# Kernel optimization log

Measured on AMD Instinct MI355X. Metric: run time of the kernel, lower is better.

## Reference

```python
import jax, jax.numpy as jnp
import numpy as np

N_SUM, N_MAX, M, HID, OUT, E, L = 2048, 64, 16, 128, 64, 16384, 4


def setup_inputs() -> dict:
    key = jax.random.key(0)
    ks = jax.random.split(key, 8)
    inp = {}
    inp["W"] = jax.random.normal(ks[0], (N_SUM, N_MAX, M), jnp.float32)
    inp["mask"] = jnp.ones((N_SUM, N_MAX), jnp.float32)
    inp["src"] = jax.random.randint(ks[1], (E,), 0, N_SUM)
    inp["dst"] = jax.random.randint(ks[2], (E,), 0, N_SUM)
    # GIN parameters: per-layer eps, MLP (Linear -> BN -> ReLU -> Linear)
    inp["eps"] = jax.random.normal(ks[3], (L,), jnp.float32)
    inp["W1_first"] = jax.random.normal(ks[4], (M, HID), jnp.float32) / np.sqrt(M).astype(np.float32)
    inp["b1_first"] = jnp.zeros((HID,), jnp.float32)
    inp["W1_rest"] = jax.random.normal(ks[5], (L - 1, HID, HID), jnp.float32) / np.sqrt(HID).astype(np.float32)
    inp["b1_rest"] = jnp.zeros((L - 1, HID), jnp.float32)
    inp["bn_gamma"] = jnp.ones((L, HID), jnp.float32)
    inp["bn_beta"] = jnp.zeros((L, HID), jnp.float32)
    inp["W2_mid"] = jax.random.normal(ks[6], (L - 1, HID, HID), jnp.float32) / np.sqrt(HID).astype(np.float32)
    inp["b2_mid"] = jnp.zeros((L - 1, HID), jnp.float32)
    inp["W2_last"] = jax.random.normal(ks[7], (HID, OUT), jnp.float32) / np.sqrt(HID).astype(np.float32)
    inp["b2_last"] = jnp.zeros((OUT,), jnp.float32)
    return inp


def _batchnorm(Hf, gamma, beta):
    # training-mode BatchNorm1d over flattened leading dims (biased variance)
    mu = Hf.mean(axis=0)
    var = Hf.var(axis=0)
    return (Hf - mu) * jax.lax.rsqrt(var + 1e-5) * gamma + beta


def _gin_layer(X, src, dst, eps, W1, b1, gamma, beta, W2, b2):
    # scatter-add message passing: gather sources, segment-sum into targets
    S = jax.ops.segment_sum(X[src], dst, num_segments=X.shape[0])  # [N_sum, n_max, D]
    Z = (1.0 + eps) * X + S
    H = Z @ W1 + b1                     # [N_sum, n_max, HID]
    shp = H.shape
    H = _batchnorm(H.reshape(-1, shp[-1]), gamma, beta)
    H = jax.nn.relu(H).reshape(shp)
    return H @ W2 + b2


def reference(W, mask, src, dst, eps, W1_first, b1_first, W1_rest, b1_rest,
              bn_gamma, bn_beta, W2_mid, b2_mid, W2_last, b2_last):
    X = W
    for l in range(L):
        W1 = W1_first if l == 0 else W1_rest[l - 1]
        b1 = b1_first if l == 0 else b1_rest[l - 1]
        W2 = W2_mid[l] if l < L - 1 else W2_last
        b2 = b2_mid[l] if l < L - 1 else b2_last
        X = _gin_layer(X, src, dst, eps[l], W1, b1, bn_gamma[l], bn_beta[l], W2, b2)
    # masked sum over the padded node axis -> positional encodings [N_sum, OUT]
    PE = (X * mask[:, :, None]).sum(axis=1)
    return PE
```

## Files before the change

kernel.cpp:

```cpp
#include <hip/hip_runtime.h>

#define N_SUM 2048
#define HIDD 128
#define NEDGE 16384
#define ROWS (N_SUM * 64)
#define NSLOT 16

typedef short short8 __attribute__((ext_vector_type(8)));
typedef float floatx4 __attribute__((ext_vector_type(4)));
typedef unsigned int uint4n __attribute__((ext_vector_type(4)));
typedef unsigned short ushort_t;

__device__ __forceinline__ ushort_t f2bf(float f) {
    unsigned u = __builtin_bit_cast(unsigned, f);
    u += 0x7fffu + ((u >> 16) & 1u);
    return (ushort_t)(u >> 16);
}
__device__ __forceinline__ float bf2f(ushort_t h) {
    return __builtin_bit_cast(float, (unsigned)h << 16);
}
__device__ __forceinline__ void unpack8(uint4 v, float* f) {
    f[0] = bf2f(v.x & 0xffff); f[1] = bf2f(v.x >> 16);
    f[2] = bf2f(v.y & 0xffff); f[3] = bf2f(v.y >> 16);
    f[4] = bf2f(v.z & 0xffff); f[5] = bf2f(v.z >> 16);
    f[6] = bf2f(v.w & 0xffff); f[7] = bf2f(v.w >> 16);
}
__device__ __forceinline__ uint4 pack8(const float* f) {
    uint4 v;
    v.x = f2bf(f[0]) | ((unsigned)f2bf(f[1]) << 16);
    v.y = f2bf(f[2]) | ((unsigned)f2bf(f[3]) << 16);
    v.z = f2bf(f[4]) | ((unsigned)f2bf(f[5]) << 16);
    v.w = f2bf(f[6]) | ((unsigned)f2bf(f[7]) << 16);
    return v;
}
__device__ __forceinline__ void nt_store16(const void* src, void* dst) {
    __builtin_nontemporal_store(*(const uint4n*)src, (uint4n*)dst);
}

__global__ __launch_bounds__(256) void zero_ints(int* p, int n) {
    int i = blockIdx.x * 256 + threadIdx.x;
    if (i < n) p[i] = 0;
}

__global__ __launch_bounds__(256) void count_deg(const int* __restrict__ dst, int* __restrict__ deg) {
    int e = blockIdx.x * 256 + threadIdx.x;
    if (e < NEDGE) atomicAdd(&deg[dst[e]], 1);
}

__global__ __launch_bounds__(256) void scan_deg(const int* __restrict__ deg, int* __restrict__ row_ptr) {
    __shared__ int csum[256];
    int t = threadIdx.x;
    int loc[8];
    int s = 0;
#pragma unroll
    for (int q = 0; q < 8; q++) { loc[q] = s; s += deg[t * 8 + q]; }
    csum[t] = s;
    __syncthreads();
    for (int off = 1; off < 256; off <<= 1) {
        int v = (t >= off) ? csum[t - off] : 0;
        __syncthreads();
        csum[t] += v;
        __syncthreads();
    }
    int base = (t == 0) ? 0 : csum[t - 1];
#pragma unroll
    for (int q = 0; q < 8; q++) row_ptr[t * 8 + q] = base + loc[q];
    if (t == 255) row_ptr[2048] = csum[255];
}

__global__ __launch_bounds__(256) void fill_csr(const int* __restrict__ src, const int* __restrict__ dst,
                                                const int* __restrict__ row_ptr, int* __restrict__ cursor,
                                                int* __restrict__ col) {
    int e = blockIdx.x * 256 + threadIdx.x;
    if (e < NEDGE) {
        int d = dst[e];
        int pos = atomicAdd(&cursor[d], 1);
        col[row_ptr[d] + pos] = src[e];
    }
}

__global__ __launch_bounds__(256) void prep_small(const float* __restrict__ W1f, const float* __restrict__ W2l,
                                                  const float* __restrict__ b2m, const float* __restrict__ W1r,
                                                  ushort_t* __restrict__ w1t0, ushort_t* __restrict__ w2lt,
                                                  float* __restrict__ bvec) {
    int idx = blockIdx.x * 256 + threadIdx.x;
    if (idx < 4096) {
        int nn = idx >> 5, k = idx & 31;
        w1t0[idx] = f2bf(k < 16 ? W1f[k * 128 + nn] : 0.f);
    } else if (idx < 4096 + 8192) {
        int r = idx - 4096;
        int nn = r >> 7, k = r & 127;
        w2lt[r] = f2bf(W2l[k * 64 + nn]);
    } else if (idx < 4096 + 8192 + 384) {
        int r = idx - 12288;
        int lm = r >> 7, c = r & 127;
        float s = 0.f;
        for (int o = 0; o < 128; o++) s += b2m[lm * 128 + o] * W1r[(size_t)lm * 16384 + o * 128 + c];
        bvec[r] = s;
    }
}

__global__ __launch_bounds__(256) void prep_w21(const float* __restrict__ W2m, const float* __restrict__ W1r,
                                                ushort_t* __restrict__ w21t) {
    int idx = blockIdx.x * 256 + threadIdx.x;
    int lm = idx >> 14, r = idx & 16383, i = r >> 7, c = r & 127;
    const float* w2row = W2m + (size_t)lm * 16384 + i * 128;
    const float* w1col = W1r + (size_t)lm * 16384 + c;
    float s = 0.f;
#pragma unroll 8
    for (int o = 0; o < 128; o++) s += w2row[o] * w1col[o * 128];
    w21t[(size_t)lm * 16384 + c * 128 + i] = f2bf(s);
}


__global__ __launch_bounds__(256, 4) void gin_mm1_l0(const float* __restrict__ Xf, const ushort_t* __restrict__ W1t,
                                                     const float* __restrict__ b1, const float* __restrict__ eps,
                                                     const int* __restrict__ rp, const int* __restrict__ colv,
                                                     ushort_t* __restrict__ H, float* __restrict__ sums) {
    __shared__ ushort_t Zs[64 * 128];
    int tid = threadIdx.x, n = blockIdx.x;
    float ev = 1.0f + eps[0];
    int e0 = rp[n], e1 = rp[n + 1], deg = e1 - e0;
    const float4* X = (const float4*)Xf;

    float4 sA, sB;
    sA = X[(size_t)n * 256 + tid];
    if (deg > 0) sB = X[(size_t)colv[e0] * 256 + tid];
    float4 a;
    a.x = sA.x * ev; a.y = sA.y * ev; a.z = sA.z * ev; a.w = sA.w * ev;
    int i = 1;
    for (; i + 1 < deg; i += 2) {
        sA = X[(size_t)colv[e0 + i] * 256 + tid];
        a.x += sB.x; a.y += sB.y; a.z += sB.z; a.w += sB.w;
        sB = X[(size_t)colv[e0 + i + 1] * 256 + tid];
        a.x += sA.x; a.y += sA.y; a.z += sA.z; a.w += sA.w;
    }
    if (deg > 0) {
        if (i < deg) {
            sA = X[(size_t)colv[e0 + i] * 256 + tid];
            a.x += sB.x; a.y += sB.y; a.z += sB.z; a.w += sB.w;
            a.x += sA.x; a.y += sA.y; a.z += sA.z; a.w += sA.w;
        } else {
            a.x += sB.x; a.y += sB.y; a.z += sB.z; a.w += sB.w;
        }
    }

    {
        int m = tid >> 2, k0 = (tid & 3) * 4;
        int addr = ((k0 >> 3) * 64 + m) * 8 + (k0 & 7);
        uint2 pv;
        pv.x = f2bf(a.x) | ((unsigned)f2bf(a.y) << 16);
        pv.y = f2bf(a.z) | ((unsigned)f2bf(a.w) << 16);
        *(uint2*)&Zs[addr] = pv;
        *(uint2*)&Zs[1024 + tid * 4] = make_uint2(0u, 0u);
    }
    __syncthreads();

    int w = tid >> 6, lane = tid & 63, lg = lane >> 4, ln = lane & 15;
    floatx4 C[4][2];
#pragma unroll
    for (int mt = 0; mt < 4; mt++) { C[mt][0] = {0.f, 0.f, 0.f, 0.f}; C[mt][1] = {0.f, 0.f, 0.f, 0.f}; }

    {
        short8 B0 = *(const short8*)&W1t[(w * 32 + ln) * 32 + lg * 8];
        short8 B1 = *(const short8*)&W1t[(w * 32 + 16 + ln) * 32 + lg * 8];
#pragma unroll
        for (int mt = 0; mt < 4; mt++) {
            short8 A = *(const short8*)&Zs[(lg * 64 + mt * 16 + ln) * 8];
            C[mt][0] = __builtin_amdgcn_mfma_f32_16x16x32_bf16(A, B0, C[mt][0], 0, 0, 0);
            C[mt][1] = __builtin_amdgcn_mfma_f32_16x16x32_bf16(A, B1, C[mt][1], 0, 0, 0);
        }
    }

    float bsum[2], bsq[2];
    float bv[2] = {b1[w * 32 + ln], b1[w * 32 + 16 + ln]};
#pragma unroll
    for (int nt = 0; nt < 2; nt++) {
        float s = 0.f, s2 = 0.f;
#pragma unroll
        for (int mt = 0; mt < 4; mt++)
#pragma unroll
            for (int r = 0; r < 4; r++) {
                float v = C[mt][nt][r] + bv[nt];
                C[mt][nt][r] = v;
                s += v; s2 += v * v;
            }
        bsum[nt] = s; bsq[nt] = s2;
    }
#pragma unroll
    for (int nt = 0; nt < 2; nt++) {
        bsum[nt] += __shfl_xor(bsum[nt], 16, 64);
        bsum[nt] += __shfl_xor(bsum[nt], 32, 64);
        bsq[nt] += __shfl_xor(bsq[nt], 16, 64);
        bsq[nt] += __shfl_xor(bsq[nt], 32, 64);
    }
    if (lg == 0) {
        float* sl = sums + (n & (NSLOT - 1)) * 256;
        int c0 = w * 32 + ln;
        atomicAdd(&sl[c0], bsum[0]);
        atomicAdd(&sl[c0 + 16], bsum[1]);
        atomicAdd(&sl[128 + c0], bsq[0]);
        atomicAdd(&sl[128 + c0 + 16], bsq[1]);
    }
    __syncthreads();
#pragma unroll
    for (int nt = 0; nt < 2; nt++) {
        int colc = w * 32 + nt * 16 + ln;
        int base = (colc >> 3) * 512 + (colc & 7);
#pragma unroll
        for (int mt = 0; mt < 4; mt++)
#pragma unroll
            for (int r = 0; r < 4; r++) {
                int row = mt * 16 + lg * 4 + r;
                Zs[base + row * 8] = f2bf(C[mt][nt][r]);
            }
    }
    __syncthreads();
#pragma unroll
    for (int q = 0; q < 4; q++)
        nt_store16(&((const uint4*)Zs)[q * 256 + tid], &((uint4*)&H[(size_t)n * 8192])[q * 256 + tid]);
}

__global__ __launch_bounds__(512, 4) void gin_mm1_fused(const ushort_t* __restrict__ Hin,
                                                        const ushort_t* __restrict__ W21t,
                                                        const float* __restrict__ b1, const float* __restrict__ bvec,
                                                        const float* __restrict__ sums_prev,
                                                        const float* __restrict__ gam_prev,
                                                        const float* __restrict__ bet_prev,
                                                        const float* __restrict__ epsp,
                                                        const int* __restrict__ rp, const int* __restrict__ colv,
                                                        ushort_t* __restrict__ Hout, float* __restrict__ sums_cur) {
    __shared__ ushort_t Zs[64 * 128];
    __shared__ float scs_lds[256];
    int tid = threadIdx.x, n = blockIdx.x;
    if (tid < 128) {
        float s = 0.f, s2 = 0.f;
#pragma unroll
        for (int k = 0; k < NSLOT; k++) {
            s += sums_prev[k * 256 + tid];
            s2 += sums_prev[k * 256 + 128 + tid];
        }
        float mean = s * (1.f / (float)ROWS);
        float var = s2 * (1.f / (float)ROWS) - mean * mean;
        float sc = gam_prev[tid] * rsqrtf(var + 1e-5f);
        scs_lds[tid] = sc;
        scs_lds[128 + tid] = bet_prev[tid] - mean * sc;
    }
    __syncthreads();

    unsigned scp[2][8];
#pragma unroll
    for (int q = 0; q < 2; q++) {
        int cb = ((q * 512 + tid) >> 6) * 8;
#pragma unroll
        for (int j = 0; j < 8; j++)
            scp[q][j] = ((unsigned)f2bf(scs_lds[cb + j])) | ((unsigned)f2bf(scs_lds[128 + cb + j]) << 16);
    }

    float ev = 1.0f + epsp[0];
    int e0 = rp[n], e1 = rp[n + 1], deg = e1 - e0;
    const uint4* X = (const uint4*)Hin;
    float acc[2][8];
    uint4 bufA[2], bufB[2];

    auto loadslab = [&](uint4* buf, int node) {
        const uint4* p = X + (size_t)node * 1024;
        buf[0] = p[tid];
        buf[1] = p[512 + tid];
    };
    auto addp = [&](const uint4* buf) {
#pragma unroll
        for (int q = 0; q < 2; q++) {
            float f[8]; unpack8(buf[q], f);
#pragma unroll
            for (int j = 0; j < 8; j++) {
                float sc = __builtin_bit_cast(float, scp[q][j] << 16);
                float sh = __builtin_bit_cast(float, scp[q][j] & 0xffff0000u);
                acc[q][j] += fmaxf(fmaf(f[j], sc, sh), 0.f);
            }
        }
    };

    loadslab(bufA, n);
    if (deg > 0) loadslab(bufB, colv[e0]);

#pragma unroll
    for (int q = 0; q < 2; q++) {
        float f[8]; unpack8(bufA[q], f);
#pragma unroll
        for (int j = 0; j < 8; j++) {
            float sc = __builtin_bit_cast(float, scp[q][j] << 16);
            float sh = __builtin_bit_cast(float, scp[q][j] & 0xffff0000u);
            acc[q][j] = ev * fmaxf(fmaf(f[j], sc, sh), 0.f);
        }
    }

    int i = 1;
    for (; i + 1 < deg; i += 2) {
        loadslab(bufA, colv[e0 + i]);
        addp(bufB);
        loadslab(bufB, colv[e0 + i + 1]);
        addp(bufA);
    }
    if (deg > 0) {
        if (i < deg) {
            loadslab(bufA, colv[e0 + i]);
            addp(bufB);
            addp(bufA);
        } else {
            addp(bufB);
        }
    }

#pragma unroll
    for (int q = 0; q < 2; q++) ((uint4*)Zs)[q * 512 + tid] = pack8(acc[q]);
    __syncthreads();

    int w = tid >> 6, lane = tid & 63, lg = lane >> 4, ln = lane & 15;
    floatx4 C[4];
#pragma unroll
    for (int mt = 0; mt < 4; mt++) C[mt] = {0.f, 0.f, 0.f, 0.f};

    for (int kb = 0; kb < 4; kb++) {
        short8 B = *(const short8*)&W21t[(w * 16 + ln) * 128 + kb * 32 + lg * 8];
#pragma unroll
        for (int mt = 0; mt < 4; mt++) {
            short8 A = *(const short8*)&Zs[((kb * 4 + lg) * 64 + mt * 16 + ln) * 8];
            C[mt] = __builtin_amdgcn_mfma_f32_16x16x32_bf16(A, B, C[mt], 0, 0, 0);
        }
    }

    float fac = ev + (float)deg;
    int c0 = w * 16 + ln;
    float bv = b1[c0] + fac * bvec[c0];
    float s = 0.f, s2 = 0.f;
#pragma unroll
    for (int mt = 0; mt < 4; mt++)
#pragma unroll
        for (int r = 0; r < 4; r++) {
            float v = C[mt][r] + bv;
            C[mt][r] = v;
            s += v; s2 += v * v;
        }
    s += __shfl_xor(s, 16, 64);
    s += __shfl_xor(s, 32, 64);
    s2 += __shfl_xor(s2, 16, 64);
    s2 += __shfl_xor(s2, 32, 64);
    if (lg == 0) {
        float* sl = sums_cur + (n & (NSLOT - 1)) * 256;
        atomicAdd(&sl[c0], s);
        atomicAdd(&sl[128 + c0], s2);
    }

    __syncthreads();
    {
        int base = (c0 >> 3) * 512 + (c0 & 7);
#pragma unroll
        for (int mt = 0; mt < 4; mt++)
#pragma unroll
            for (int r = 0; r < 4; r++) {
                int row = mt * 16 + lg * 4 + r;
                Zs[base + row * 8] = f2bf(C[mt][r]);
            }
    }
    __syncthreads();
#pragma unroll
    for (int q = 0; q < 2; q++)
        nt_store16(&((const uint4*)Zs)[q * 512 + tid], &((uint4*)&Hout[(size_t)n * 8192])[q * 512 + tid]);
}

__global__ __launch_bounds__(256, 4) void gin_mm2_last(const ushort_t* __restrict__ H, const ushort_t* __restrict__ W2t,
                                                       const float* __restrict__ b2,
                                                       const float* __restrict__ sums_prev,
                                                       const float* __restrict__ gam_prev,
                                                       const float* __restrict__ bet_prev,
                                                       const float* __restrict__ mask, float* __restrict__ out) {
    __shared__ ushort_t Hs[64 * 128];
    __shared__ float scs_lds[256];
    int tid = threadIdx.x, n = blockIdx.x;
    if (tid < 128) {
        float s = 0.f, s2 = 0.f;
#pragma unroll
        for (int k = 0; k < NSLOT; k++) {
            s += sums_prev[k * 256 + tid];
            s2 += sums_prev[k * 256 + 128 + tid];
        }
        float mean = s * (1.f / (float)ROWS);
        float var = s2 * (1.f / (float)ROWS) - mean * mean;
        float sc = gam_prev[tid] * rsqrtf(var + 1e-5f);
        scs_lds[tid] = sc;
        scs_lds[128 + tid] = bet_prev[tid] - mean * sc;
    }
    __syncthreads();

#pragma unroll
    for (int q = 0; q < 4; q++) {
        int c = q * 256 + tid;
        uint4 v = ((const uint4*)&H[(size_t)n * 8192])[c];
        float f[8]; unpack8(v, f);
        int cb = (c >> 6) * 8;
#pragma unroll
        for (int j = 0; j < 8; j++) f[j] = fmaxf(fmaf(f[j], scs_lds[cb + j], scs_lds[128 + cb + j]), 0.f);
        ((uint4*)Hs)[c] = pack8(f);
    }
    __syncthreads();

    int w = tid >> 6, lane = tid & 63, lg = lane >> 4, ln = lane & 15;
    floatx4 C[4];
#pragma unroll
    for (int mt = 0; mt < 4; mt++) C[mt] = {0.f, 0.f, 0.f, 0.f};

    for (int kb = 0; kb < 4; kb++) {
        short8 B = *(const short8*)&W2t[(w * 16 + ln) * 128 + kb * 32 + lg * 8];
#pragma unroll
        for (int mt = 0; mt < 4; mt++) {
            short8 A = *(const short8*)&Hs[((kb * 4 + lg) * 64 + mt * 16 + ln) * 8];
            C[mt] = __builtin_amdgcn_mfma_f32_16x16x32_bf16(A, B, C[mt], 0, 0, 0);
        }
    }

    int colc = w * 16 + ln;
    float bb = b2[colc];
    float pe = 0.f;
#pragma unroll
    for (int mt = 0; mt < 4; mt++)
#pragma unroll
        for (int r = 0; r < 4; r++) {
            int row = mt * 16 + lg * 4 + r;
            pe += mask[n * 64 + row] * (C[mt][r] + bb);
        }
    pe += __shfl_xor(pe, 16, 64);
    pe += __shfl_xor(pe, 32, 64);
    if (lg == 0) out[(size_t)n * 64 + colc] = pe;
}

extern "C" void kernel_launch(void* const* d_in, const int* in_sizes, int n_in, void* d_out, int out_size,
                              void* d_ws, size_t ws_size, hipStream_t stream) {
    const float* W    = (const float*)d_in[0];
    const float* mask = (const float*)d_in[1];
    const int* src    = (const int*)d_in[2];
    const int* dst    = (const int*)d_in[3];
    const float* eps  = (const float*)d_in[4];
    const float* W1f  = (const float*)d_in[5];
    const float* b1f  = (const float*)d_in[6];
    const float* W1r  = (const float*)d_in[7];
    const float* b1r  = (const float*)d_in[8];
    const float* gam  = (const float*)d_in[9];
    const float* bet  = (const float*)d_in[10];
    const float* W2m  = (const float*)d_in[11];
    const float* b2m  = (const float*)d_in[12];
    const float* W2l  = (const float*)d_in[13];
    const float* b2l  = (const float*)d_in[14];
    float* out = (float*)d_out;

    ushort_t* Ha   = (ushort_t*)d_ws;
    ushort_t* Hb   = Ha + 16777216;
    ushort_t* w1t0 = Hb + 16777216;
    ushort_t* w2lt = w1t0 + 4096;
    ushort_t* w21t = w2lt + 8192;
    float* bvec    = (float*)(w21t + 49152);
    int* ideg      = (int*)(bvec + 384);
    int* icur      = ideg + 2048;
    float* sums    = (float*)(icur + 2048);
    int* irp       = (int*)(sums + 16384);
    int* icol      = irp + 2052;

    zero_ints<<<80, 256, 0, stream>>>(ideg, 20480);
    count_deg<<<NEDGE / 256, 256, 0, stream>>>(dst, ideg);
    scan_deg<<<1, 256, 0, stream>>>(ideg, irp);
    fill_csr<<<NEDGE / 256, 256, 0, stream>>>(src, dst, irp, icur, icol);
    prep_small<<<50, 256, 0, stream>>>(W1f, W2l, b2m, W1r, w1t0, w2lt, bvec);
    prep_w21<<<192, 256, 0, stream>>>(W2m, W1r, w21t);

    gin_mm1_l0<<<N_SUM, 256, 0, stream>>>(W, w1t0, b1f, eps, irp, icol, Ha, sums);
    gin_mm1_fused<<<N_SUM, 512, 0, stream>>>(Ha, w21t, b1r, bvec, sums, gam, bet, eps + 1,
                                             irp, icol, Hb, sums + NSLOT * 256);
    gin_mm1_fused<<<N_SUM, 512, 0, stream>>>(Hb, w21t + 16384, b1r + 128, bvec + 128, sums + NSLOT * 256,
                                             gam + 128, bet + 128, eps + 2, irp, icol, Ha, sums + 2 * NSLOT * 256);
    gin_mm1_fused<<<N_SUM, 512, 0, stream>>>(Ha, w21t + 32768, b1r + 256, bvec + 256, sums + 2 * NSLOT * 256,
                                             gam + 256, bet + 256, eps + 3, irp, icol, Hb, sums + 3 * NSLOT * 256);
    gin_mm2_last<<<N_SUM, 256, 0, stream>>>(Hb, w2lt, b2l, sums + 3 * NSLOT * 256, gam + 384, bet + 384, mask, out);
}
```

Measured before the change: 273.4 us.

## Merge preprocessing kernels and split fused GIN layer blocks across two halves

```diff
diff --git a/kernel.cpp b/kernel.cpp
--- a/kernel.cpp
+++ b/kernel.cpp
@@ -4,7 +4,7 @@
 #define HIDD 128
 #define NEDGE 16384
 #define ROWS (N_SUM * 64)
-#define NSLOT 16
+#define NSLOT 32
 
 typedef short short8 __attribute__((ext_vector_type(8)));
 typedef float floatx4 __attribute__((ext_vector_type(4)));
@@ -37,79 +37,80 @@
     __builtin_nontemporal_store(*(const uint4n*)src, (uint4n*)dst);
 }
 
-__global__ __launch_bounds__(256) void zero_ints(int* p, int n) {
-    int i = blockIdx.x * 256 + threadIdx.x;
-    if (i < n) p[i] = 0;
-}
-
-__global__ __launch_bounds__(256) void count_deg(const int* __restrict__ dst, int* __restrict__ deg) {
-    int e = blockIdx.x * 256 + threadIdx.x;
-    if (e < NEDGE) atomicAdd(&deg[dst[e]], 1);
-}
-
-__global__ __launch_bounds__(256) void scan_deg(const int* __restrict__ deg, int* __restrict__ row_ptr) {
+__global__ __launch_bounds__(256) void mega_prep(const int* __restrict__ src, const int* __restrict__ dst,
+                                                 const float* __restrict__ W1f, const float* __restrict__ W2l,
+                                                 const float* __restrict__ b2m, const float* __restrict__ W1r,
+                                                 const float* __restrict__ W2m,
+                                                 int* __restrict__ irp, int* __restrict__ icol,
+                                                 ushort_t* __restrict__ w1t0, ushort_t* __restrict__ w2lt,
+                                                 float* __restrict__ bvec, ushort_t* __restrict__ w21t,
+                                                 float* __restrict__ sums) {
+    __shared__ int sdeg[2048];
+    __shared__ int scur[2048];
     __shared__ int csum[256];
-    int t = threadIdx.x;
-    int loc[8];
-    int s = 0;
-#pragma unroll
-    for (int q = 0; q < 8; q++) { loc[q] = s; s += deg[t * 8 + q]; }
-    csum[t] = s;
-    __syncthreads();
-    for (int off = 1; off < 256; off <<= 1) {
-        int v = (t >= off) ? csum[t - off] : 0;
+    int tid = threadIdx.x, blk = blockIdx.x;
+
+    if (blk == 0) {
+        for (int i = tid; i < 2048; i += 256) sdeg[i] = 0;
         __syncthreads();
-        csum[t] += v;
+        for (int e = tid; e < NEDGE; e += 256) atomicAdd(&sdeg[dst[e]], 1);
         __syncthreads();
-    }
-    int base = (t == 0) ? 0 : csum[t - 1];
-#pragma unroll
-    for (int q = 0; q < 8; q++) row_ptr[t * 8 + q] = base + loc[q];
-    if (t == 255) row_ptr[2048] = csum[255];
-}
-
-__global__ __launch_bounds__(256) void fill_csr(const int* __restrict__ src, const int* __restrict__ dst,
-                                                const int* __restrict__ row_ptr, int* __restrict__ cursor,
-                                                int* __restrict__ col) {
-    int e = blockIdx.x * 256 + threadIdx.x;
-    if (e < NEDGE) {
-        int d = dst[e];
-        int pos = atomicAdd(&cursor[d], 1);
-        col[row_ptr[d] + pos] = src[e];
-    }
-}
-
-__global__ __launch_bounds__(256) void prep_small(const float* __restrict__ W1f, const float* __restrict__ W2l,
-                                                  const float* __restrict__ b2m, const float* __restrict__ W1r,
-                                                  ushort_t* __restrict__ w1t0, ushort_t* __restrict__ w2lt,
-                                                  float* __restrict__ bvec) {
-    int idx = blockIdx.x * 256 + threadIdx.x;
-    if (idx < 4096) {
-        int nn = idx >> 5, k = idx & 31;
-        w1t0[idx] = f2bf(k < 16 ? W1f[k * 128 + nn] : 0.f);
-    } else if (idx < 4096 + 8192) {
-        int r = idx - 4096;
-        int nn = r >> 7, k = r & 127;
-        w2lt[r] = f2bf(W2l[k * 64 + nn]);
-    } else if (idx < 4096 + 8192 + 384) {
-        int r = idx - 12288;
-        int lm = r >> 7, c = r & 127;
+        int loc[8], s = 0;
+#pragma unroll
+        for (int q = 0; q < 8; q++) { loc[q] = s; s += sdeg[tid * 8 + q]; }
+        csum[tid] = s;
+        __syncthreads();
+        for (int off = 1; off < 256; off <<= 1) {
+            int v = (tid >= off) ? csum[tid - off] : 0;
+            __syncthreads();
+            csum[tid] += v;
+            __syncthreads();
+        }
+        int base = (tid == 0) ? 0 : csum[tid - 1];
+#pragma unroll
+        for (int q = 0; q < 8; q++) {
+            int node = tid * 8 + q;
+            int rpv = base + loc[q];
+            irp[node] = rpv;
+            scur[node] = rpv;
+        }
+        if (tid == 255) irp[2048] = csum[255];
+        __syncthreads();
+        for (int e = tid; e < NEDGE; e += 256) {
+            int d = dst[e];
+            int pos = atomicAdd(&scur[d], 1);
+            icol[pos] = src[e];
+        }
+    } else if (blk <= 50) {
+        int idx = (blk - 1) * 256 + tid;
+        if (idx < 4096) {
+            int nn = idx >> 5, k = idx & 31;
+            w1t0[idx] = f2bf(k < 16 ? W1f[k * 128 + nn] : 0.f);
+        } else if (idx < 4096 + 8192) {
+            int r = idx - 4096;
+            int nn = r >> 7, k = r & 127;
+            w2lt[r] = f2bf(W2l[k * 64 + nn]);
+        } else if (idx < 4096 + 8192 + 384) {
+            int r = idx - 12288;
+            int lm = r >> 7, c = r & 127;
+            float s = 0.f;
+            for (int o = 0; o < 128; o++) s += b2m[lm * 128 + o] * W1r[(size_t)lm * 16384 + o * 128 + c];
+            bvec[r] = s;
+        }
+    } else if (blk <= 242) {
+        int idx = (blk - 51) * 256 + tid;
+        int lm = idx >> 14, r = idx & 16383, i = r >> 7, c = r & 127;
+        const float* w2row = W2m + (size_t)lm * 16384 + i * 128;
+        const float* w1col = W1r + (size_t)lm * 16384 + c;
         float s = 0.f;
-        for (int o = 0; o < 128; o++) s += b2m[lm * 128 + o] * W1r[(size_t)lm * 16384 + o * 128 + c];
-        bvec[r] = s;
-    }
-}
-
-__global__ __launch_bounds__(256) void prep_w21(const float* __restrict__ W2m, const float* __restrict__ W1r,
-                                                ushort_t* __restrict__ w21t) {
-    int idx = blockIdx.x * 256 + threadIdx.x;
-    int lm = idx >> 14, r = idx & 16383, i = r >> 7, c = r & 127;
-    const float* w2row = W2m + (size_t)lm * 16384 + i * 128;
-    const float* w1col = W1r + (size_t)lm * 16384 + c;
-    float s = 0.f;
 #pragma unroll 8
-    for (int o = 0; o < 128; o++) s += w2row[o] * w1col[o * 128];
-    w21t[(size_t)lm * 16384 + c * 128 + i] = f2bf(s);
+        for (int o = 0; o < 128; o++) s += w2row[o] * w1col[o * 128];
+        w21t[(size_t)lm * 16384 + c * 128 + i] = f2bf(s);
+    } else {
+        int idx = (blk - 243) * 256 + tid;
+#pragma unroll
+        for (int q = 0; q < 8; q++) sums[idx * 8 + q] = 0.f;
+    }
 }
 
 
@@ -221,7 +222,7 @@
         nt_store16(&((const uint4*)Zs)[q * 256 + tid], &((uint4*)&H[(size_t)n * 8192])[q * 256 + tid]);
 }
 
-__global__ __launch_bounds__(512, 4) void gin_mm1_fused(const ushort_t* __restrict__ Hin,
+__global__ __launch_bounds__(256, 6) void gin_mm1_fused(const ushort_t* __restrict__ Hin,
                                                         const ushort_t* __restrict__ W21t,
                                                         const float* __restrict__ b1, const float* __restrict__ bvec,
                                                         const float* __restrict__ sums_prev,
@@ -230,9 +231,11 @@
                                                         const float* __restrict__ epsp,
                                                         const int* __restrict__ rp, const int* __restrict__ colv,
                                                         ushort_t* __restrict__ Hout, float* __restrict__ sums_cur) {
-    __shared__ ushort_t Zs[64 * 128];
+    __shared__ ushort_t Zs[32 * 128];
     __shared__ float scs_lds[256];
-    int tid = threadIdx.x, n = blockIdx.x;
+    int tid = threadIdx.x;
+    int n = blockIdx.x >> 1, h = blockIdx.x & 1;
+
     if (tid < 128) {
         float s = 0.f, s2 = 0.f;
 #pragma unroll
@@ -251,7 +254,7 @@
     unsigned scp[2][8];
 #pragma unroll
     for (int q = 0; q < 2; q++) {
-        int cb = ((q * 512 + tid) >> 6) * 8;
+        int cb = ((q * 256 + tid) >> 5) * 8;
 #pragma unroll
         for (int j = 0; j < 8; j++)
             scp[q][j] = ((unsigned)f2bf(scs_lds[cb + j])) | ((unsigned)f2bf(scs_lds[128 + cb + j]) << 16);
@@ -260,13 +263,14 @@
     float ev = 1.0f + epsp[0];
     int e0 = rp[n], e1 = rp[n + 1], deg = e1 - e0;
     const uint4* X = (const uint4*)Hin;
+    int off = (tid >> 5) * 64 + (tid & 31);
     float acc[2][8];
     uint4 bufA[2], bufB[2];
 
     auto loadslab = [&](uint4* buf, int node) {
-        const uint4* p = X + (size_t)node * 1024;
-        buf[0] = p[tid];
-        buf[1] = p[512 + tid];
+        const uint4* p = X + (size_t)node * 1024 + h * 32;
+        buf[0] = p[off];
+        buf[1] = p[512 + off];
     };
     auto addp = [&](const uint4* buf) {
 #pragma unroll
@@ -312,61 +316,82 @@
         }
     }
 
-#pragma unroll
-    for (int q = 0; q < 2; q++) ((uint4*)Zs)[q * 512 + tid] = pack8(acc[q]);
+    {
+        int pos0 = (tid >> 5) * 32 + (tid & 31);
+        ((uint4*)Zs)[pos0] = pack8(acc[0]);
+        ((uint4*)Zs)[256 + pos0] = pack8(acc[1]);
+    }
     __syncthreads();
 
     int w = tid >> 6, lane = tid & 63, lg = lane >> 4, ln = lane & 15;
-    floatx4 C[4];
-#pragma unroll
-    for (int mt = 0; mt < 4; mt++) C[mt] = {0.f, 0.f, 0.f, 0.f};
+    floatx4 C[2][2];
+#pragma unroll
+    for (int mt = 0; mt < 2; mt++) { C[mt][0] = {0.f, 0.f, 0.f, 0.f}; C[mt][1] = {0.f, 0.f, 0.f, 0.f}; }
 
     for (int kb = 0; kb < 4; kb++) {
-        short8 B = *(const short8*)&W21t[(w * 16 + ln) * 128 + kb * 32 + lg * 8];
-#pragma unroll
-        for (int mt = 0; mt < 4; mt++) {
-            short8 A = *(const short8*)&Zs[((kb * 4 + lg) * 64 + mt * 16 + ln) * 8];
-            C[mt] = __builtin_amdgcn_mfma_f32_16x16x32_bf16(A, B, C[mt], 0, 0, 0);
+        short8 B0 = *(const short8*)&W21t[(w * 32 + ln) * 128 + kb * 32 + lg * 8];
+        short8 B1 = *(const short8*)&W21t[(w * 32 + 16 + ln) * 128 + kb * 32 + lg * 8];
+#pragma unroll
+        for (int mt = 0; mt < 2; mt++) {
+            short8 A = *(const short8*)&Zs[((kb * 4 + lg) * 32 + mt * 16 + ln) * 8];
+            C[mt][0] = __builtin_amdgcn_mfma_f32_16x16x32_bf16(A, B0, C[mt][0], 0, 0, 0);
+            C[mt][1] = __builtin_amdgcn_mfma_f32_16x16x32_bf16(A, B1, C[mt][1], 0, 0, 0);
         }
     }
 
     float fac = ev + (float)deg;
-    int c0 = w * 16 + ln;
-    float bv = b1[c0] + fac * bvec[c0];
-    float s = 0.f, s2 = 0.f;
-#pragma unroll
-    for (int mt = 0; mt < 4; mt++)
-#pragma unroll
-        for (int r = 0; r < 4; r++) {
-            float v = C[mt][r] + bv;
-            C[mt][r] = v;
-            s += v; s2 += v * v;
-        }
-    s += __shfl_xor(s, 16, 64);
-    s += __shfl_xor(s, 32, 64);
-    s2 += __shfl_xor(s2, 16, 64);
-    s2 += __shfl_xor(s2, 32, 64);
+    float bsum[2], bsq[2];
+    float bv[2] = {b1[w * 32 + ln] + fac * bvec[w * 32 + ln],
+                   b1[w * 32 + 16 + ln] + fac * bvec[w * 32 + 16 + ln]};
+#pragma unroll
+    for (int nt = 0; nt < 2; nt++) {
+        float s = 0.f, s2 = 0.f;
+#pragma unroll
+        for (int mt = 0; mt < 2; mt++)
+#pragma unroll
+            for (int r = 0; r < 4; r++) {
+                float v = C[mt][nt][r] + bv[nt];
+                C[mt][nt][r] = v;
+                s += v; s2 += v * v;
+            }
+        bsum[nt] = s; bsq[nt] = s2;
+    }
+#pragma unroll
+    for (int nt = 0; nt < 2; nt++) {
+        bsum[nt] += __shfl_xor(bsum[nt], 16, 64);
+        bsum[nt] += __shfl_xor(bsum[nt], 32, 64);
+        bsq[nt] += __shfl_xor(bsq[nt], 16, 64);
+        bsq[nt] += __shfl_xor(bsq[nt], 32, 64);
+    }
     if (lg == 0) {
-        float* sl = sums_cur + (n & (NSLOT - 1)) * 256;
-        atomicAdd(&sl[c0], s);
-        atomicAdd(&sl[128 + c0], s2);
-    }
-
+        float* sl = sums_cur + (blockIdx.x & (NSLOT - 1)) * 256;
+        int c0 = w * 32 + ln;
+        atomicAdd(&sl[c0], bsum[0]);
+        atomicAdd(&sl[c0 + 16], bsum[1]);
+        atomicAdd(&sl[128 + c0], bsq[0]);
+        atomicAdd(&sl[128 + c0 + 16], bsq[1]);
+    }
+
+    __syncthreads();
+#pragma unroll
+    for (int nt = 0; nt < 2; nt++) {
+        int colc = w * 32 + nt * 16 + ln;
+        int base = (colc >> 3) * 256 + (colc & 7);
+#pragma unroll
+        for (int mt = 0; mt < 2; mt++)
+#pragma unroll
+            for (int r = 0; r < 4; r++) {
+                int mh = mt * 16 + lg * 4 + r;
+                Zs[base + mh * 8] = f2bf(C[mt][nt][r]);
+            }
+    }
     __syncthreads();
     {
-        int base = (c0 >> 3) * 512 + (c0 & 7);
-#pragma unroll
-        for (int mt = 0; mt < 4; mt++)
-#pragma unroll
-            for (int r = 0; r < 4; r++) {
-                int row = mt * 16 + lg * 4 + r;
-                Zs[base + row * 8] = f2bf(C[mt][r]);
-            }
-    }
-    __syncthreads();
-#pragma unroll
-    for (int q = 0; q < 2; q++)
-        nt_store16(&((const uint4*)Zs)[q * 512 + tid], &((uint4*)&Hout[(size_t)n * 8192])[q * 512 + tid]);
+        int pos0 = (tid >> 5) * 32 + (tid & 31);
+        uint4* Hd = (uint4*)&Hout[(size_t)n * 8192];
+        nt_store16(&((const uint4*)Zs)[pos0], &Hd[off + h * 32]);
+        nt_store16(&((const uint4*)Zs)[256 + pos0], &Hd[512 + off + h * 32]);
+    }
 }
 
 __global__ __launch_bounds__(256, 4) void gin_mm2_last(const ushort_t* __restrict__ H, const ushort_t* __restrict__ W2t,
@@ -459,25 +484,20 @@
     ushort_t* w2lt = w1t0 + 4096;
     ushort_t* w21t = w2lt + 8192;
     float* bvec    = (float*)(w21t + 49152);
-    int* ideg      = (int*)(bvec + 384);
-    int* icur      = ideg + 2048;
-    float* sums    = (float*)(icur + 2048);
-    int* irp       = (int*)(sums + 16384);
+    float* sums    = bvec + 384;
+    int* irp       = (int*)(sums + 32768);
     int* icol      = irp + 2052;
 
-    zero_ints<<<80, 256, 0, stream>>>(ideg, 20480);
-    count_deg<<<NEDGE / 256, 256, 0, stream>>>(dst, ideg);
-    scan_deg<<<1, 256, 0, stream>>>(ideg, irp);
-    fill_csr<<<NEDGE / 256, 256, 0, stream>>>(src, dst, irp, icur, icol);
-    prep_small<<<50, 256, 0, stream>>>(W1f, W2l, b2m, W1r, w1t0, w2lt, bvec);
-    prep_w21<<<192, 256, 0, stream>>>(W2m, W1r, w21t);
-
+    mega_prep<<<259, 256, 0, stream>>>(src, dst, W1f, W2l, b2m, W1r, W2m, irp, icol,
+                                       w1t0, w2lt, bvec, w21t, sums);
+
+    const int SL = NSLOT * 256;
     gin_mm1_l0<<<N_SUM, 256, 0, stream>>>(W, w1t0, b1f, eps, irp, icol, Ha, sums);
-    gin_mm1_fused<<<N_SUM, 512, 0, stream>>>(Ha, w21t, b1r, bvec, sums, gam, bet, eps + 1,
-                                             irp, icol, Hb, sums + NSLOT * 256);
-    gin_mm1_fused<<<N_SUM, 512, 0, stream>>>(Hb, w21t + 16384, b1r + 128, bvec + 128, sums + NSLOT * 256,
-                                             gam + 128, bet + 128, eps + 2, irp, icol, Ha, sums + 2 * NSLOT * 256);
-    gin_mm1_fused<<<N_SUM, 512, 0, stream>>>(Ha, w21t + 32768, b1r + 256, bvec + 256, sums + 2 * NSLOT * 256,
-                                             gam + 256, bet + 256, eps + 3, irp, icol, Hb, sums + 3 * NSLOT * 256);
-    gin_mm2_last<<<N_SUM, 256, 0, stream>>>(Hb, w2lt, b2l, sums + 3 * NSLOT * 256, gam + 384, bet + 384, mask, out);
-}
+    gin_mm1_fused<<<2 * N_SUM, 256, 0, stream>>>(Ha, w21t, b1r, bvec, sums, gam, bet, eps + 1,
+                                                 irp, icol, Hb, sums + SL);
+    gin_mm1_fused<<<2 * N_SUM, 256, 0, stream>>>(Hb, w21t + 16384, b1r + 128, bvec + 128, sums + SL,
+                                                 gam + 128, bet + 128, eps + 2, irp, icol, Ha, sums + 2 * SL);
+    gin_mm1_fused<<<2 * N_SUM, 256, 0, stream>>>(Ha, w21t + 32768, b1r + 256, bvec + 256, sums + 2 * SL,
+                                                 gam + 256, bet + 256, eps + 3, irp, icol, Hb, sums + 3 * SL);
+    gin_mm2_last<<<N_SUM, 256, 0, stream>>>(Hb, w2lt, b2l, sums + 3 * SL, gam + 384, bet + 384, mask, out);
+}
```

New measurement: 330.0 us. 1.21x slower.

## Merge graph CSR build and weight preprocessing into one multi-role kernel

Applied to the files above, without the earlier changes.

```diff
diff --git a/kernel.cpp b/kernel.cpp
--- a/kernel.cpp
+++ b/kernel.cpp
@@ -37,79 +37,83 @@
     __builtin_nontemporal_store(*(const uint4n*)src, (uint4n*)dst);
 }
 
-__global__ __launch_bounds__(256) void zero_ints(int* p, int n) {
-    int i = blockIdx.x * 256 + threadIdx.x;
-    if (i < n) p[i] = 0;
-}
-
-__global__ __launch_bounds__(256) void count_deg(const int* __restrict__ dst, int* __restrict__ deg) {
-    int e = blockIdx.x * 256 + threadIdx.x;
-    if (e < NEDGE) atomicAdd(&deg[dst[e]], 1);
-}
-
-__global__ __launch_bounds__(256) void scan_deg(const int* __restrict__ deg, int* __restrict__ row_ptr) {
-    __shared__ int csum[256];
-    int t = threadIdx.x;
-    int loc[8];
-    int s = 0;
-#pragma unroll
-    for (int q = 0; q < 8; q++) { loc[q] = s; s += deg[t * 8 + q]; }
-    csum[t] = s;
-    __syncthreads();
-    for (int off = 1; off < 256; off <<= 1) {
-        int v = (t >= off) ? csum[t - off] : 0;
+__global__ __launch_bounds__(1024) void mega_prep(const int* __restrict__ src, const int* __restrict__ dst,
+                                                  const float* __restrict__ W1f, const float* __restrict__ W2l,
+                                                  const float* __restrict__ b2m, const float* __restrict__ W1r,
+                                                  const float* __restrict__ W2m,
+                                                  int* __restrict__ irp, int* __restrict__ icol,
+                                                  ushort_t* __restrict__ w1t0, ushort_t* __restrict__ w2lt,
+                                                  float* __restrict__ bvec, ushort_t* __restrict__ w21t,
+                                                  float* __restrict__ sums) {
+    __shared__ int sdeg[2048];
+    __shared__ int scur[2048];
+    __shared__ int red[1024];
+    int tid = threadIdx.x, blk = blockIdx.x;
+
+    if (blk == 0) {
+        sdeg[tid] = 0;
+        sdeg[tid + 1024] = 0;
         __syncthreads();
-        csum[t] += v;
+        int d[16];
+#pragma unroll
+        for (int q = 0; q < 16; q++) d[q] = dst[q * 1024 + tid];
+#pragma unroll
+        for (int q = 0; q < 16; q++) atomicAdd(&sdeg[d[q]], 1);
         __syncthreads();
-    }
-    int base = (t == 0) ? 0 : csum[t - 1];
-#pragma unroll
-    for (int q = 0; q < 8; q++) row_ptr[t * 8 + q] = base + loc[q];
-    if (t == 255) row_ptr[2048] = csum[255];
-}
-
-__global__ __launch_bounds__(256) void fill_csr(const int* __restrict__ src, const int* __restrict__ dst,
-                                                const int* __restrict__ row_ptr, int* __restrict__ cursor,
-                                                int* __restrict__ col) {
-    int e = blockIdx.x * 256 + threadIdx.x;
-    if (e < NEDGE) {
-        int d = dst[e];
-        int pos = atomicAdd(&cursor[d], 1);
-        col[row_ptr[d] + pos] = src[e];
-    }
-}
-
-__global__ __launch_bounds__(256) void prep_small(const float* __restrict__ W1f, const float* __restrict__ W2l,
-                                                  const float* __restrict__ b2m, const float* __restrict__ W1r,
-                                                  ushort_t* __restrict__ w1t0, ushort_t* __restrict__ w2lt,
-                                                  float* __restrict__ bvec) {
-    int idx = blockIdx.x * 256 + threadIdx.x;
-    if (idx < 4096) {
-        int nn = idx >> 5, k = idx & 31;
-        w1t0[idx] = f2bf(k < 16 ? W1f[k * 128 + nn] : 0.f);
-    } else if (idx < 4096 + 8192) {
-        int r = idx - 4096;
-        int nn = r >> 7, k = r & 127;
-        w2lt[r] = f2bf(W2l[k * 64 + nn]);
-    } else if (idx < 4096 + 8192 + 384) {
-        int r = idx - 12288;
-        int lm = r >> 7, c = r & 127;
+        int a = sdeg[2 * tid], b = sdeg[2 * tid + 1];
+        red[tid] = a + b;
+        __syncthreads();
+        for (int off = 1; off < 1024; off <<= 1) {
+            int v = (tid >= off) ? red[tid - off] : 0;
+            __syncthreads();
+            red[tid] += v;
+            __syncthreads();
+        }
+        int base = (tid == 0) ? 0 : red[tid - 1];
+        irp[2 * tid] = base;
+        irp[2 * tid + 1] = base + a;
+        scur[2 * tid] = base;
+        scur[2 * tid + 1] = base + a;
+        if (tid == 1023) irp[2048] = red[1023];
+        __syncthreads();
+        int s[16];
+#pragma unroll
+        for (int q = 0; q < 16; q++) s[q] = src[q * 1024 + tid];
+#pragma unroll
+        for (int q = 0; q < 16; q++) {
+            int pos = atomicAdd(&scur[d[q]], 1);
+            icol[pos] = s[q];
+        }
+    } else if (blk <= 13) {
+        int idx = (blk - 1) * 1024 + tid;
+        if (idx < 4096) {
+            int nn = idx >> 5, k = idx & 31;
+            w1t0[idx] = f2bf(k < 16 ? W1f[k * 128 + nn] : 0.f);
+        } else if (idx < 4096 + 8192) {
+            int r = idx - 4096;
+            int nn = r >> 7, k = r & 127;
+            w2lt[r] = f2bf(W2l[k * 64 + nn]);
+        } else if (idx < 4096 + 8192 + 384) {
+            int r = idx - 12288;
+            int lm = r >> 7, c = r & 127;
+            float s = 0.f;
+            for (int o = 0; o < 128; o++) s += b2m[lm * 128 + o] * W1r[(size_t)lm * 16384 + o * 128 + c];
+            bvec[r] = s;
+        }
+    } else if (blk <= 61) {
+        int idx = (blk - 14) * 1024 + tid;
+        int lm = idx >> 14, r = idx & 16383, i = r >> 7, c = r & 127;
+        const float* w2row = W2m + (size_t)lm * 16384 + i * 128;
+        const float* w1col = W1r + (size_t)lm * 16384 + c;
         float s = 0.f;
-        for (int o = 0; o < 128; o++) s += b2m[lm * 128 + o] * W1r[(size_t)lm * 16384 + o * 128 + c];
-        bvec[r] = s;
-    }
-}
-
-__global__ __launch_bounds__(256) void prep_w21(const float* __restrict__ W2m, const float* __restrict__ W1r,
-                                                ushort_t* __restrict__ w21t) {
-    int idx = blockIdx.x * 256 + threadIdx.x;
-    int lm = idx >> 14, r = idx & 16383, i = r >> 7, c = r & 127;
-    const float* w2row = W2m + (size_t)lm * 16384 + i * 128;
-    const float* w1col = W1r + (size_t)lm * 16384 + c;
-    float s = 0.f;
 #pragma unroll 8
-    for (int o = 0; o < 128; o++) s += w2row[o] * w1col[o * 128];
-    w21t[(size_t)lm * 16384 + c * 128 + i] = f2bf(s);
+        for (int o = 0; o < 128; o++) s += w2row[o] * w1col[o * 128];
+        w21t[(size_t)lm * 16384 + c * 128 + i] = f2bf(s);
+    } else {
+        int idx = (blk - 62) * 1024 + tid;
+#pragma unroll
+        for (int q = 0; q < 8; q++) sums[idx * 8 + q] = 0.f;
+    }
 }
 
 
@@ -459,25 +463,20 @@
     ushort_t* w2lt = w1t0 + 4096;
     ushort_t* w21t = w2lt + 8192;
     float* bvec    = (float*)(w21t + 49152);
-    int* ideg      = (int*)(bvec + 384);
-    int* icur      = ideg + 2048;
-    float* sums    = (float*)(icur + 2048);
+    float* sums    = bvec + 384;
     int* irp       = (int*)(sums + 16384);
     int* icol      = irp + 2052;
 
-    zero_ints<<<80, 256, 0, stream>>>(ideg, 20480);
-    count_deg<<<NEDGE / 256, 256, 0, stream>>>(dst, ideg);
-    scan_deg<<<1, 256, 0, stream>>>(ideg, irp);
-    fill_csr<<<NEDGE / 256, 256, 0, stream>>>(src, dst, irp, icur, icol);
-    prep_small<<<50, 256, 0, stream>>>(W1f, W2l, b2m, W1r, w1t0, w2lt, bvec);
-    prep_w21<<<192, 256, 0, stream>>>(W2m, W1r, w21t);
-
+    mega_prep<<<64, 1024, 0, stream>>>(src, dst, W1f, W2l, b2m, W1r, W2m, irp, icol,
+                                       w1t0, w2lt, bvec, w21t, sums);
+
+    const int SL = NSLOT * 256;
     gin_mm1_l0<<<N_SUM, 256, 0, stream>>>(W, w1t0, b1f, eps, irp, icol, Ha, sums);
     gin_mm1_fused<<<N_SUM, 512, 0, stream>>>(Ha, w21t, b1r, bvec, sums, gam, bet, eps + 1,
-                                             irp, icol, Hb, sums + NSLOT * 256);
-    gin_mm1_fused<<<N_SUM, 512, 0, stream>>>(Hb, w21t + 16384, b1r + 128, bvec + 128, sums + NSLOT * 256,
-                                             gam + 128, bet + 128, eps + 2, irp, icol, Ha, sums + 2 * NSLOT * 256);
-    gin_mm1_fused<<<N_SUM, 512, 0, stream>>>(Ha, w21t + 32768, b1r + 256, bvec + 256, sums + 2 * NSLOT * 256,
-                                             gam + 256, bet + 256, eps + 3, irp, icol, Hb, sums + 3 * NSLOT * 256);
-    gin_mm2_last<<<N_SUM, 256, 0, stream>>>(Hb, w2lt, b2l, sums + 3 * NSLOT * 256, gam + 384, bet + 384, mask, out);
-}
+                                             irp, icol, Hb, sums + SL);
+    gin_mm1_fused<<<N_SUM, 512, 0, stream>>>(Hb, w21t + 16384, b1r + 128, bvec + 128, sums + SL,
+                                             gam + 128, bet + 128, eps + 2, irp, icol, Ha, sums + 2 * SL);
+    gin_mm1_fused<<<N_SUM, 512, 0, stream>>>(Ha, w21t + 32768, b1r + 256, bvec + 256, sums + 2 * SL,
+                                             gam + 256, bet + 256, eps + 3, irp, icol, Hb, sums + 3 * SL);
+    gin_mm2_last<<<N_SUM, 256, 0, stream>>>(Hb, w2lt, b2l, sums + 3 * SL, gam + 384, bet + 384, mask, out);
+}
```

After: 263.7 us. 1.04x faster.
